# Kernel tuning notes

Measured on AMD Instinct MI355X. Metric: run time of the kernel, lower is better.

The kernel has to match this reference:

```python
import jax, jax.numpy as jnp
import numpy as np

H_BEV, W_BEV, Z_LEVELS = 240, 120, 6  # BEV grid; length = Z_LEVELS*H_BEV*W_BEV = 172800


def setup_inputs() -> dict:
    key = jax.random.key(0)
    ks = jax.random.split(key, 7)
    C, H, W = 64, 256, 448
    L = Z_LEVELS * H_BEV * W_BEV  # 172800 voxels
    fish_input = jax.random.normal(ks[0], (1, 4, C, H, W), dtype=jnp.float32)
    pv_input = jax.random.normal(ks[1], (1, 1, C, H, W), dtype=jnp.float32)
    front_input = jax.random.normal(ks[2], (1, 1, C, H, W), dtype=jnp.float32)
    uu = jax.random.randint(ks[3], (6, L), 0, W)
    vv = jax.random.randint(ks[4], (6, L), 0, H)
    valid = jax.random.randint(ks[5], (6, L), 0, 2)
    density = jax.random.uniform(ks[6], (6, L), dtype=jnp.float32)
    return {"fish_input": fish_input, "pv_input": pv_input, "front_input": front_input,
            "uu": uu, "vv": vv, "valid": valid, "density": density}


def reference(fish_input, pv_input, front_input, uu, vv, valid, density):
    # Concatenate cameras: [6, C, H, W]
    feats = jnp.concatenate([fish_input[0], pv_input[0], front_input[0]], axis=0)
    n_cam, C, H, W = feats.shape
    L = uu.shape[1]
    # Gather per-voxel pixel features: flatten spatial, index by vv*W+uu
    flat = feats.reshape(n_cam, C, H * W)                 # [6, C, H*W]
    pix = (vv * W + uu).astype(jnp.int32)                 # [6, L]
    gathered = jnp.take_along_axis(flat, pix[:, None, :], axis=2)  # [6, C, L]
    # Validity mask + density weighting
    w = valid.astype(feats.dtype) * density               # [6, L]
    weighted = gathered * w[:, None, :]                   # [6, C, L]
    # Scatter-accumulate: voxels are z-major over BEV cells -> sum the Z levels per cell
    bev = weighted.reshape(n_cam, C, Z_LEVELS, H_BEV * W_BEV).sum(axis=2)
    return bev.reshape(1, n_cam * C, H_BEV, W_BEV)        # [1, 384, 240, 120]
```

## Files before the change

### kernel.cpp

```cpp
#include <hip/hip_runtime.h>
#include <hip/hip_fp16.h>

#define HW_PIX  114688
#define W_IMG   448
#define C_CH    64
#define NCAM    6
#define NCELL   28800
#define ZL      6
#define LVOX    172800
#define TILE_PX 256
#define NTILES  (HW_PIX / TILE_PX)

__global__ __launch_bounds__(256) void vp_transpose_q8(
    const float* __restrict__ fish, const float* __restrict__ pv,
    const float* __restrict__ front,
    signed char* __restrict__ featsQ, float* __restrict__ scaleArr)
{
    const int bid  = blockIdx.x;
    const int cam  = bid / NTILES;
    const int tile = bid % NTILES;
    const int pix0 = tile * TILE_PX;

    const float* src = (cam < 4) ? (fish + (size_t)cam * C_CH * HW_PIX)
                                 : ((cam == 4) ? pv : front);

    __shared__ __half t[64][260];
    __shared__ float  wmax[4];

    const int tid = threadIdx.x;
    const int w   = tid >> 6;
    const int l   = tid & 63;

    float m = 0.0f;
    #pragma unroll
    for (int i = 0; i < 16; ++i) {
        const int c = w * 16 + i;
        const float4 f = *reinterpret_cast<const float4*>(
            src + (size_t)c * HW_PIX + pix0 + l * 4);
        m = fmaxf(m, fmaxf(fmaxf(fabsf(f.x), fabsf(f.y)),
                           fmaxf(fabsf(f.z), fabsf(f.w))));
        __half2 h01 = __floats2half2_rn(f.x, f.y);
        __half2 h23 = __floats2half2_rn(f.z, f.w);
        *reinterpret_cast<__half2*>(&t[c][l * 4 + 0]) = h01;
        *reinterpret_cast<__half2*>(&t[c][l * 4 + 2]) = h23;
    }

    #pragma unroll
    for (int o = 32; o > 0; o >>= 1) m = fmaxf(m, __shfl_xor(m, o));
    if (l == 0) wmax[w] = m;
    __syncthreads();
    const float tmax = fmaxf(fmaxf(wmax[0], wmax[1]), fmaxf(wmax[2], wmax[3]));
    const float inv  = (tmax > 0.0f) ? (127.0f / tmax) : 0.0f;
    if (tid == 0) scaleArr[cam * NTILES + tile] = tmax * (1.0f / 127.0f);

    signed char* dstc = featsQ + ((size_t)cam * HW_PIX + pix0) * 64;
    #pragma unroll
    for (int it = 0; it < 4; ++it) {
        const int e    = it * 256 + tid;
        const int pair = e >> 3;
        const int g    = e & 7;
        const int px   = pair * 2;
        uint2 o0, o1;
        o0.x = o0.y = o1.x = o1.y = 0u;
        #pragma unroll
        for (int k = 0; k < 8; ++k) {
            const __half2 h2 = *reinterpret_cast<const __half2*>(
                &t[g * 8 + k][px]);
            const float v0 = __low2float(h2);
            const float v1 = __high2float(h2);
            int q0 = (int)rintf(v0 * inv);
            int q1 = (int)rintf(v1 * inv);
            q0 = q0 > 127 ? 127 : (q0 < -127 ? -127 : q0);
            q1 = q1 > 127 ? 127 : (q1 < -127 ? -127 : q1);
            const unsigned int b0 = (unsigned int)(q0 & 0xff);
            const unsigned int b1 = (unsigned int)(q1 & 0xff);
            if (k < 4) { o0.x |= b0 << (8 * k);       o1.x |= b1 << (8 * k); }
            else       { o0.y |= b0 << (8 * (k - 4)); o1.y |= b1 << (8 * (k - 4)); }
        }
        signed char* dp = dstc + (size_t)px * 64 + g * 8;
        *reinterpret_cast<uint2*>(dp)      = o0;
        *reinterpret_cast<uint2*>(dp + 64) = o1;
    }
}

__global__ __launch_bounds__(256) void vp_gather_q8(
    const signed char* __restrict__ featsQ, const float* __restrict__ scaleArr,
    const int*   __restrict__ uu, const int* __restrict__ vv,
    const int*   __restrict__ valid, const float* __restrict__ density,
    float* __restrict__ out)
{
    const int bid   = blockIdx.x;
    const int cam   = bid / (NCELL / 64);
    const int cell0 = (bid % (NCELL / 64)) * 64;
    const int tid   = threadIdx.x;

    __shared__ int   p_s[ZL * 64];
    __shared__ float w_s[ZL * 64];
    __shared__ float s_scale[NTILES];
    __shared__ float acc_s[64][65];

    for (int j = tid; j < NTILES; j += 256)
        s_scale[j] = scaleArr[cam * NTILES + j];
    for (int v = tid; v < ZL * 64; v += 256) {
        int z  = v >> 6;
        int cl = v & 63;
        size_t l = (size_t)cam * LVOX + (size_t)z * NCELL + cell0 + cl;
        p_s[v] = vv[l] * W_IMG + uu[l];
        w_s[v] = valid[l] ? density[l] : 0.0f;
    }
    __syncthreads();

    const int g  = tid >> 3;
    const int la = tid & 7;
    const signed char* base = featsQ + (size_t)cam * HW_PIX * 64 + la * 8;

    float acc[2][8];
    #pragma unroll
    for (int ci = 0; ci < 2; ++ci)
        #pragma unroll
        for (int k = 0; k < 8; ++k) acc[ci][k] = 0.0f;

    #pragma unroll
    for (int ci = 0; ci < 2; ++ci) {
        const int cl = g + ci * 32;
        #pragma unroll
        for (int z = 0; z < ZL; ++z) {
            const int v = z * 64 + cl;
            const float w = w_s[v];
            if (w != 0.0f) {
                const int p = p_s[v];
                const uint2 q = *reinterpret_cast<const uint2*>(
                    base + (size_t)p * 64);
                const float sw = w * s_scale[p >> 8];
                acc[ci][0] += (float)((int)(signed char)(q.x      )) * sw;
                acc[ci][1] += (float)((int)(signed char)(q.x >>  8)) * sw;
                acc[ci][2] += (float)((int)(signed char)(q.x >> 16)) * sw;
                acc[ci][3] += (float)((int)(signed char)(q.x >> 24)) * sw;
                acc[ci][4] += (float)((int)(signed char)(q.y      )) * sw;
                acc[ci][5] += (float)((int)(signed char)(q.y >>  8)) * sw;
                acc[ci][6] += (float)((int)(signed char)(q.y >> 16)) * sw;
                acc[ci][7] += (float)((int)(signed char)(q.y >> 24)) * sw;
            }
        }
    }

    #pragma unroll
    for (int ci = 0; ci < 2; ++ci) {
        const int cl = g + ci * 32;
        #pragma unroll
        for (int k = 0; k < 8; ++k)
            acc_s[cl][la * 8 + k] = acc[ci][k];
    }
    __syncthreads();

    #pragma unroll
    for (int i = 0; i < 4; ++i) {
        int e   = i * 256 + tid;
        int c   = e >> 4;
        int cl4 = e & 15;
        float4 f;
        f.x = acc_s[cl4 * 4 + 0][c];
        f.y = acc_s[cl4 * 4 + 1][c];
        f.z = acc_s[cl4 * 4 + 2][c];
        f.w = acc_s[cl4 * 4 + 3][c];
        *reinterpret_cast<float4*>(
            out + ((size_t)cam * C_CH + c) * NCELL + cell0 + cl4 * 4) = f;
    }
}

__global__ __launch_bounds__(256) void vp_fallback_kernel(
    const float* __restrict__ fish, const float* __restrict__ pv,
    const float* __restrict__ front,
    const int*   __restrict__ uu, const int* __restrict__ vv,
    const int*   __restrict__ valid, const float* __restrict__ density,
    float* __restrict__ out)
{
    const int idx = blockIdx.x * 256 + threadIdx.x;
    if (idx >= NCAM * C_CH * NCELL) return;
    const int cell = idx % NCELL;
    const int c    = (idx / NCELL) % C_CH;
    const int cam  = idx / (NCELL * C_CH);
    const float* src = (cam < 4)
        ? (fish + ((size_t)cam * C_CH + c) * HW_PIX)
        : (((cam == 4) ? pv : front) + (size_t)c * HW_PIX);
    float acc = 0.0f;
    for (int z = 0; z < ZL; ++z) {
        const size_t l = (size_t)cam * LVOX + (size_t)z * NCELL + cell;
        if (valid[l]) {
            acc += src[vv[l] * W_IMG + uu[l]] * density[l];
        }
    }
    out[idx] = acc;
}

extern "C" void kernel_launch(void* const* d_in, const int* in_sizes, int n_in,
                              void* d_out, int out_size, void* d_ws, size_t ws_size,
                              hipStream_t stream) {
    const float* fish    = (const float*)d_in[0];
    const float* pv      = (const float*)d_in[1];
    const float* front   = (const float*)d_in[2];
    const int*   uu      = (const int*)d_in[3];
    const int*   vv      = (const int*)d_in[4];
    const int*   valid   = (const int*)d_in[5];
    const float* density = (const float*)d_in[6];
    float*       out     = (float*)d_out;

    const size_t featsBytes = (size_t)NCAM * HW_PIX * 64;
    const size_t need = featsBytes + (size_t)NCAM * NTILES * sizeof(float);

    if (ws_size >= need) {
        signed char* featsQ  = (signed char*)d_ws;
        float*       scaleArr = (float*)((char*)d_ws + featsBytes);
        vp_transpose_q8<<<NCAM * NTILES, 256, 0, stream>>>(
            fish, pv, front, featsQ, scaleArr);
        vp_gather_q8<<<NCAM * (NCELL / 64), 256, 0, stream>>>(
            featsQ, scaleArr, uu, vv, valid, density, out);
    } else {
        vp_fallback_kernel<<<(NCAM * C_CH * NCELL + 255) / 256, 256, 0, stream>>>(
            fish, pv, front, uu, vv, valid, density, out);
    }
}
```

Baseline: 64.89 us.

## Skip quantized writes for pixels no voxel references; nontemporal output stores

A new pre-pass kernel reads the valid, uu and vv arrays and marks each image pixel that some valid voxel samples in a per-camera byte mask. The transpose/quantize kernel loads this mask per tile and skips computing and storing int8 features for unreferenced pixels, cutting writes to the workspace. The gather kernel's output stores become nontemporal vector stores. In exchange, the pre-pass adds a full extra read of the index arrays, scattered byte writes and an extra launch. The mask is never cleared, so stale entries only cause redundant writes and do not affect correctness.

```diff
diff --git a/kernel.cpp b/kernel.cpp
--- a/kernel.cpp
+++ b/kernel.cpp
@@ -11,9 +11,23 @@
 #define TILE_PX 256
 #define NTILES  (HW_PIX / TILE_PX)
 
+typedef float vfloat4 __attribute__((ext_vector_type(4)));
+
+__global__ __launch_bounds__(256) void vp_coverage(
+    const int* __restrict__ uu, const int* __restrict__ vv,
+    const int* __restrict__ valid, unsigned char* __restrict__ mask)
+{
+    const int idx = blockIdx.x * 256 + threadIdx.x;
+    if (idx >= NCAM * LVOX) return;
+    if (valid[idx]) {
+        const int cam = idx / LVOX;
+        mask[(size_t)cam * HW_PIX + vv[idx] * W_IMG + uu[idx]] = 1;
+    }
+}
+
 __global__ __launch_bounds__(256) void vp_transpose_q8(
     const float* __restrict__ fish, const float* __restrict__ pv,
-    const float* __restrict__ front,
+    const float* __restrict__ front, const unsigned char* __restrict__ mask,
     signed char* __restrict__ featsQ, float* __restrict__ scaleArr)
 {
     const int bid  = blockIdx.x;
@@ -26,10 +40,15 @@
 
     __shared__ __half t[64][260];
     __shared__ float  wmax[4];
+    __shared__ unsigned int m_s[TILE_PX / 4];
 
     const int tid = threadIdx.x;
     const int w   = tid >> 6;
     const int l   = tid & 63;
+
+    if (tid < TILE_PX / 4)
+        m_s[tid] = *((const unsigned int*)(mask + (size_t)cam * HW_PIX + pix0)
+                     + tid);
 
     float m = 0.0f;
     #pragma unroll
@@ -60,6 +79,10 @@
         const int pair = e >> 3;
         const int g    = e & 7;
         const int px   = pair * 2;
+        const unsigned int wd = m_s[px >> 2] >> ((px & 2) * 8);
+        const bool c0 = (wd & 0x000000ffu) == 1u;
+        const bool c1 = (wd & 0x0000ff00u) == 0x100u;
+        if (!(c0 | c1)) continue;
         uint2 o0, o1;
         o0.x = o0.y = o1.x = o1.y = 0u;
         #pragma unroll
@@ -78,8 +101,8 @@
             else       { o0.y |= b0 << (8 * (k - 4)); o1.y |= b1 << (8 * (k - 4)); }
         }
         signed char* dp = dstc + (size_t)px * 64 + g * 8;
-        *reinterpret_cast<uint2*>(dp)      = o0;
-        *reinterpret_cast<uint2*>(dp + 64) = o1;
+        if (c0) *reinterpret_cast<uint2*>(dp)      = o0;
+        if (c1) *reinterpret_cast<uint2*>(dp + 64) = o1;
     }
 }
 
@@ -158,13 +181,13 @@
         int e   = i * 256 + tid;
         int c   = e >> 4;
         int cl4 = e & 15;
-        float4 f;
+        vfloat4 f;
         f.x = acc_s[cl4 * 4 + 0][c];
         f.y = acc_s[cl4 * 4 + 1][c];
         f.z = acc_s[cl4 * 4 + 2][c];
         f.w = acc_s[cl4 * 4 + 3][c];
-        *reinterpret_cast<float4*>(
-            out + ((size_t)cam * C_CH + c) * NCELL + cell0 + cl4 * 4) = f;
+        __builtin_nontemporal_store(f, reinterpret_cast<vfloat4*>(
+            out + ((size_t)cam * C_CH + c) * NCELL + cell0 + cl4 * 4));
     }
 }
 
@@ -206,13 +229,18 @@
     float*       out     = (float*)d_out;
 
     const size_t featsBytes = (size_t)NCAM * HW_PIX * 64;
-    const size_t need = featsBytes + (size_t)NCAM * NTILES * sizeof(float);
+    const size_t scaleBytes = (size_t)NCAM * NTILES * sizeof(float);
+    const size_t maskBytes  = (size_t)NCAM * HW_PIX;
+    const size_t need = featsBytes + scaleBytes + maskBytes;
 
     if (ws_size >= need) {
-        signed char* featsQ  = (signed char*)d_ws;
-        float*       scaleArr = (float*)((char*)d_ws + featsBytes);
+        signed char*   featsQ   = (signed char*)d_ws;
+        float*         scaleArr = (float*)((char*)d_ws + featsBytes);
+        unsigned char* mask     = (unsigned char*)((char*)d_ws + featsBytes + scaleBytes);
+        vp_coverage<<<(NCAM * LVOX + 255) / 256, 256, 0, stream>>>(
+            uu, vv, valid, mask);
         vp_transpose_q8<<<NCAM * NTILES, 256, 0, stream>>>(
-            fish, pv, front, featsQ, scaleArr);
+            fish, pv, front, mask, featsQ, scaleArr);
         vp_gather_q8<<<NCAM * (NCELL / 64), 256, 0, stream>>>(
             featsQ, scaleArr, uu, vv, valid, density, out);
     } else {
```

Result: faster. 62.86 us, median of 2 (-3.1%).
